# Kernel tuning notes

Measured on AMD Instinct MI355X. Metric: run time of the kernel, lower is better.

Reference implementation:

```python
import jax, jax.numpy as jnp
import numpy as np

EPS = 1e-5

def _ln(x):
    # LayerNorm without affine (elementwise_affine=False when adaLN=True)
    m = jnp.mean(x, axis=-1, keepdims=True)
    v = jnp.mean((x - m) ** 2, axis=-1, keepdims=True)
    return (x - m) / jnp.sqrt(v + EPS)

def _ln_affine(x, g, b):
    return _ln(x) * g + b

def setup_inputs() -> dict:
    key = jax.random.key(0)
    B, L, D, H, P = 2, 1024, 1024, 16, 64
    FF = 4 * D
    ks = jax.random.split(key, 16)
    s = 0.02
    inp = {
        'x': jax.random.normal(ks[0], (B, L, D), jnp.float32),
        'z': jax.random.normal(ks[1], (B, L, L, P), jnp.float32),
        'trans': jax.random.normal(ks[2], (B, L, 3), jnp.float32),
        'mask': jnp.ones((B, L), jnp.bool_),
        'x_cond': jax.random.normal(ks[3], (B, L, D), jnp.float32),
        # adaLN modulation: SiLU -> Linear(D, 6D). (Randomly init'd; the torch
        # code zero-inits it, which would zero the whole block output.)
        'ada_W': jax.random.normal(ks[4], (D, 6 * D), jnp.float32) * s,
        'ada_b': jnp.zeros((6 * D,), jnp.float32),
        # attention projections (torch Linear weights stored as [in, out])
        'Wq': jax.random.normal(ks[5], (D, D), jnp.float32) * s,
        'bq': jnp.zeros((D,), jnp.float32),
        'Wk': jax.random.normal(ks[6], (D, D), jnp.float32) * s,
        'bk': jnp.zeros((D,), jnp.float32),
        'Wv': jax.random.normal(ks[7], (D, D), jnp.float32) * s,
        'bv': jnp.zeros((D,), jnp.float32),
        'Wo': jax.random.normal(ks[8], (D, D), jnp.float32) * s,
        'bo': jnp.zeros((D,), jnp.float32),
        # FeedForward: LayerNorm(D) (affine) -> Linear(D,FF) -> ReLU -> Linear(FF,D)
        'ln_g': jnp.ones((D,), jnp.float32),
        'ln_b': jnp.zeros((D,), jnp.float32),
        'W1': jax.random.normal(ks[9], (D, FF), jnp.float32) * s,
        'b1': jnp.zeros((FF,), jnp.float32),
        'W2': jax.random.normal(ks[10], (FF, D), jnp.float32) * s,
        'b2': jnp.zeros((D,), jnp.float32),
    }
    return inp

def _block(x, z, trans, mask, x_cond, ada_W, ada_b, Wq, bq, Wk, bk, Wv, bv,
           Wo, bo, ln_g, ln_b, W1, b1, W2, b2):
    B, L, D = x.shape
    H = 16
    dh = D // H
    # adaLN modulation from conditioning signal
    c = jax.nn.silu(x_cond) @ ada_W + ada_b
    (shift_mha, scale_mha, gate_mha,
     shift_mlp, scale_mlp, gate_mlp) = jnp.split(c, 6, axis=-1)
    # --- attention branch: norm -> modulate -> MHA -> gate -> residual ---
    h = _ln(x) * (1.0 + scale_mha) + shift_mha
    q = (h @ Wq + bq).reshape(B, L, H, dh)
    k = (h @ Wk + bk).reshape(B, L, H, dh)
    v = (h @ Wv + bv).reshape(B, L, H, dh)
    scores = jnp.einsum('blhd,bmhd->bhlm', q, k) / jnp.sqrt(jnp.float32(dh))
    neg = jnp.finfo(scores.dtype).min
    scores = jnp.where(mask[:, None, None, :], scores, neg)
    attn = jax.nn.softmax(scores, axis=-1)
    o = jnp.einsum('bhlm,bmhd->blhd', attn, v).reshape(B, L, D)
    mha_out = o @ Wo + bo
    x = x + mha_out * gate_mha
    # --- FFN branch: norm -> modulate -> FF(LN, Lin, ReLU, Lin) -> gate ---
    h = _ln(x) * (1.0 + scale_mlp) + shift_mlp
    h = _ln_affine(h, ln_g, ln_b)
    h = jax.nn.relu(h @ W1 + b1)
    ff_out = h @ W2 + b2
    x = x + ff_out * gate_mlp
    # pair_updates=False, frame_update=False: z and trans pass through
    return x, z, trans

def reference(x, z, trans, mask, x_cond, ada_W, ada_b, Wq, bq, Wk, bk, Wv, bv,
              Wo, bo, ln_g, ln_b, W1, b1, W2, b2):
    return _block(x, z, trans, mask, x_cond, ada_W, ada_b, Wq, bq, Wk, bk,
                  Wv, bv, Wo, bo, ln_g, ln_b, W1, b1, W2, b2)
```

## Files before the change

### kernel.cpp

```cpp
#include <hip/hip_runtime.h>
#include <hip/hip_bf16.h>


typedef __attribute__((ext_vector_type(8))) __bf16 bf16x8;
typedef __attribute__((ext_vector_type(4))) float f32x4;
typedef __attribute__((ext_vector_type(8))) unsigned short ushortx8;

#define DEVI static __device__ __forceinline__

DEVI unsigned short f2bf(float f) {
    __hip_bfloat16 h = __float2bfloat16(f);
    return __builtin_bit_cast(unsigned short, h);
}

DEVI void gload16(const void* g, void* l) {
    __builtin_amdgcn_global_load_lds(
        (const __attribute__((address_space(1))) void*)g,
        (__attribute__((address_space(3))) void*)l, 16, 0, 0);
}

DEVI void side_copy(const float4* __restrict__ src, float4* __restrict__ dst,
                    long long len, long long cb, long long ncb) {
    const long long nthr = ncb * 256;
    for (long long i = cb * 256 + threadIdx.x; i < len; i += nthr)
        dst[i] = src[i];
}

__global__ __launch_bounds__(256) void transpose_cast(
        const float* __restrict__ in, unsigned short* __restrict__ out,
        int K, int N) {
    __shared__ float tile[32][33];
    const int n0 = blockIdx.x * 32, k0 = blockIdx.y * 32;
    const int tx = threadIdx.x, ty = threadIdx.y;
#pragma unroll
    for (int i = 0; i < 4; ++i)
        tile[ty + 8 * i][tx] = in[(size_t)(k0 + ty + 8 * i) * N + n0 + tx];
    __syncthreads();
#pragma unroll
    for (int i = 0; i < 4; ++i)
        out[(size_t)(n0 + ty + 8 * i) * K + k0 + tx] = f2bf(tile[tx][ty + 8 * i]);
}

__global__ __launch_bounds__(256) void silu_cast(
        const float* __restrict__ x, unsigned short* __restrict__ o) {
    const int i = blockIdx.x * 256 + threadIdx.x;
    float4 v = ((const float4*)x)[i];
    ushort4 r;
    r.x = f2bf(v.x / (1.f + __expf(-v.x)));
    r.y = f2bf(v.y / (1.f + __expf(-v.y)));
    r.z = f2bf(v.z / (1.f + __expf(-v.z)));
    r.w = f2bf(v.w / (1.f + __expf(-v.w)));
    ((ushort4*)o)[i] = r;
}

__global__ void concat3(const float* __restrict__ a, const float* __restrict__ b,
                        const float* __restrict__ c, float* __restrict__ o, int D) {
    const int i = blockIdx.x * 256 + threadIdx.x;
    if (i < D) o[i] = a[i];
    else if (i < 2 * D) o[i] = b[i - D];
    else if (i < 3 * D) o[i] = c[i - 2 * D];
}

template <int MODE, int MT>
__global__ __launch_bounds__(256) void gemm_bt(
        const unsigned short* __restrict__ A, const unsigned short* __restrict__ Bt,
        const float* __restrict__ bias,
        float* __restrict__ outf, unsigned short* __restrict__ outb,
        const float* __restrict__ res, const float* __restrict__ gate, int gstride,
        int M, int N, int K,
        unsigned short* __restrict__ vt, int twoD, int H, int Lr) {
    __shared__ __align__(16) unsigned short lA[MT * 32 * 32];
    __shared__ __align__(16) unsigned short lB[128 * 32];
    const int tid = threadIdx.x;
    const int wave = tid >> 6, lane = tid & 63;
    const int fr = lane & 15, fg = lane >> 4;
    const int wr = wave >> 1, wc = wave & 1;
    const int m0 = blockIdx.y * (MT * 32), n0 = blockIdx.x * 128;

    f32x4 acc[MT][4];
#pragma unroll
    for (int i = 0; i < MT; ++i)
#pragma unroll
        for (int j = 0; j < 4; ++j) acc[i][j] = (f32x4){0.f, 0.f, 0.f, 0.f};

    for (int k0 = 0; k0 < K; k0 += 32) {
#pragma unroll
        for (int ch = 0; ch < 2; ++ch) {
            const int p = ch * 4096 + wave * 1024 + lane * 16;
            const int row = p >> 6, kb = p & 63;
            if (ch < MT / 2)
                gload16((const char*)A + ((size_t)(m0 + row) * K + k0) * 2 + kb, (char*)lA + p);
            gload16((const char*)Bt + ((size_t)(n0 + row) * K + k0) * 2 + kb, (char*)lB + p);
        }
        __syncthreads();
        bf16x8 af[MT], bfm[4];
#pragma unroll
        for (int t = 0; t < MT; ++t)
            af[t] = *(const bf16x8*)((const char*)lA + ((wr * (MT * 16) + t * 16 + fr) * 32 + fg * 8) * 2);
#pragma unroll
        for (int t = 0; t < 4; ++t)
            bfm[t] = *(const bf16x8*)((const char*)lB + ((wc * 64 + t * 16 + fr) * 32 + fg * 8) * 2);
#pragma unroll
        for (int mt = 0; mt < MT; ++mt)
#pragma unroll
            for (int nt = 0; nt < 4; ++nt)
                acc[mt][nt] = __builtin_amdgcn_mfma_f32_16x16x32_bf16(
                        af[mt], bfm[nt], acc[mt][nt], 0, 0, 0);
        __syncthreads();
    }
#pragma unroll
    for (int mt = 0; mt < MT; ++mt)
#pragma unroll
        for (int nt = 0; nt < 4; ++nt) {
            const int gcol = n0 + wc * 64 + nt * 16 + fr;
            const float bb = bias[gcol];
#pragma unroll
            for (int j = 0; j < 4; ++j) {
                const int grow = m0 + wr * (MT * 16) + mt * 16 + fg * 4 + j;
                const size_t idx = (size_t)grow * N + gcol;
                const float v = acc[mt][nt][j] + bb;
                if constexpr (MODE == 0) outf[idx] = v;
                else if constexpr (MODE == 1) outb[idx] = f2bf(v);
                else if constexpr (MODE == 2) outf[idx] = res[idx] + v * gate[(size_t)grow * gstride + gcol];
                else if constexpr (MODE == 3) outb[idx] = f2bf(fmaxf(v, 0.f));
                else {
                    const unsigned short bv16 = f2bf(v);
                    outb[idx] = bv16;
                    if (gcol >= twoD) {
                        const int d = gcol - twoD, hh = d >> 6, dd = d & 63;
                        const int bb2 = grow >= Lr ? 1 : 0, l = grow - bb2 * Lr;
                        vt[((size_t)(bb2 * H + hh) * 64 + dd) * Lr + l] = bv16;
                    }
                }
            }
        }
}

__global__ __launch_bounds__(256) void ln_mod(
        const float* __restrict__ x, const float* __restrict__ c,
        unsigned short* __restrict__ h, int D, int cs) {
    const int row = blockIdx.x, tid = threadIdx.x;
    const int lane = tid & 63, wave = tid >> 6;
    const float4 xv = ((const float4*)(x + (size_t)row * D))[tid];
    float s = xv.x + xv.y + xv.z + xv.w;
    float ss = xv.x * xv.x + xv.y * xv.y + xv.z * xv.z + xv.w * xv.w;
#pragma unroll
    for (int o = 1; o < 64; o <<= 1) { s += __shfl_xor(s, o); ss += __shfl_xor(ss, o); }
    __shared__ float red[8];
    if (lane == 0) { red[wave] = s; red[4 + wave] = ss; }
    __syncthreads();
    s = red[0] + red[1] + red[2] + red[3];
    ss = red[4] + red[5] + red[6] + red[7];
    const float mean = s / D;
    const float rstd = rsqrtf(ss / D - mean * mean + 1e-5f);
    const float* crow = c + (size_t)row * cs;
    const float4 sh = ((const float4*)(crow))[tid];
    const float4 sc = ((const float4*)(crow + D))[tid];
    ushort4 r;
    r.x = f2bf((xv.x - mean) * rstd * (1.f + sc.x) + sh.x);
    r.y = f2bf((xv.y - mean) * rstd * (1.f + sc.y) + sh.y);
    r.z = f2bf((xv.z - mean) * rstd * (1.f + sc.z) + sh.z);
    r.w = f2bf((xv.w - mean) * rstd * (1.f + sc.w) + sh.w);
    ((ushort4*)(h + (size_t)row * D))[tid] = r;
}

__global__ __launch_bounds__(256) void ln2_mod(
        const float* __restrict__ x2, const float* __restrict__ c,
        const float* __restrict__ g, const float* __restrict__ bb,
        unsigned short* __restrict__ h, int D, int cs) {
    const int row = blockIdx.x, tid = threadIdx.x;
    const int lane = tid & 63, wave = tid >> 6;
    const float4 xv = ((const float4*)(x2 + (size_t)row * D))[tid];
    float s = xv.x + xv.y + xv.z + xv.w;
    float ss = xv.x * xv.x + xv.y * xv.y + xv.z * xv.z + xv.w * xv.w;
#pragma unroll
    for (int o = 1; o < 64; o <<= 1) { s += __shfl_xor(s, o); ss += __shfl_xor(ss, o); }
    __shared__ float red[16];
    if (lane == 0) { red[wave] = s; red[4 + wave] = ss; }
    __syncthreads();
    s = red[0] + red[1] + red[2] + red[3];
    ss = red[4] + red[5] + red[6] + red[7];
    const float mean = s / D;
    const float rstd = rsqrtf(ss / D - mean * mean + 1e-5f);
    const float* crow = c + (size_t)row * cs;
    const float4 sh = ((const float4*)(crow + 3 * D))[tid];
    const float4 sc = ((const float4*)(crow + 4 * D))[tid];
    float t[4];
    t[0] = (xv.x - mean) * rstd * (1.f + sc.x) + sh.x;
    t[1] = (xv.y - mean) * rstd * (1.f + sc.y) + sh.y;
    t[2] = (xv.z - mean) * rstd * (1.f + sc.z) + sh.z;
    t[3] = (xv.w - mean) * rstd * (1.f + sc.w) + sh.w;
    float s2 = t[0] + t[1] + t[2] + t[3];
    float ss2 = t[0] * t[0] + t[1] * t[1] + t[2] * t[2] + t[3] * t[3];
#pragma unroll
    for (int o = 1; o < 64; o <<= 1) { s2 += __shfl_xor(s2, o); ss2 += __shfl_xor(ss2, o); }
    if (lane == 0) { red[8 + wave] = s2; red[12 + wave] = ss2; }
    __syncthreads();
    s2 = red[8] + red[9] + red[10] + red[11];
    ss2 = red[12] + red[13] + red[14] + red[15];
    const float mean2 = s2 / D;
    const float rstd2 = rsqrtf(ss2 / D - mean2 * mean2 + 1e-5f);
    const float4 gv = ((const float4*)g)[tid];
    const float4 bv = ((const float4*)bb)[tid];
    ushort4 r;
    r.x = f2bf((t[0] - mean2) * rstd2 * gv.x + bv.x);
    r.y = f2bf((t[1] - mean2) * rstd2 * gv.y + bv.y);
    r.z = f2bf((t[2] - mean2) * rstd2 * gv.z + bv.z);
    r.w = f2bf((t[3] - mean2) * rstd2 * gv.w + bv.w);
    ((ushort4*)(h + (size_t)row * D))[tid] = r;
}

__global__ __launch_bounds__(256) void attn_fwd(
        const unsigned short* __restrict__ qkv, const unsigned short* __restrict__ vt,
        unsigned short* __restrict__ o,
        int L, int D, int B,
        const float4* __restrict__ cp_src, float4* __restrict__ cp_dst,
        long long cp_len) {
    if ((int)blockIdx.z >= B) {
        const long long cb = (long long)(blockIdx.z - B) * gridDim.x * gridDim.y
                           + (long long)blockIdx.y * gridDim.x + blockIdx.x;
        const long long ncb = (long long)(gridDim.z - B) * gridDim.x * gridDim.y;
        side_copy(cp_src, cp_dst, cp_len, cb, ncb);
        return;
    }
    const int q0 = blockIdx.x * 64, hh = blockIdx.y, b = blockIdx.z;
    const int H = gridDim.y;
    const int tid = threadIdx.x, wave = tid >> 6, lane = tid & 63;
    const int fr = lane & 15, fg = lane >> 4;
    const size_t rs = 3 * (size_t)D;
    const unsigned short* vtb = vt + (size_t)(b * H + hh) * 64 * L;
    __shared__ __align__(16) unsigned short lK[64 * 72];
    __shared__ __align__(16) unsigned short lVT[64 * 72];
    __shared__ __align__(16) unsigned short lP[4 * 16 * 72];

    bf16x8 aq[2];
    {
        const size_t qr = (size_t)(b * L + q0 + wave * 16 + fr);
#pragma unroll
        for (int kk = 0; kk < 2; ++kk)
            aq[kk] = *(const bf16x8*)(qkv + qr * rs + hh * 64 + kk * 32 + fg * 8);
    }
    f32x4 oacc[4];
#pragma unroll
    for (int i = 0; i < 4; ++i) oacc[i] = (f32x4){0.f, 0.f, 0.f, 0.f};
    float m_run[4] = {-1e30f, -1e30f, -1e30f, -1e30f};
    float l_run[4] = {0.f, 0.f, 0.f, 0.f};

    for (int n0 = 0; n0 < L; n0 += 64) {
        __syncthreads();
#pragma unroll
        for (int it = 0; it < 2; ++it) {
            const int idx = it * 256 + tid, r = idx >> 3, cc = idx & 7;
            const unsigned short* src = qkv + (size_t)(b * L + n0 + r) * rs + D + hh * 64 + cc * 8;
            *(ushortx8*)(&lK[r * 72 + cc * 8]) = *(const ushortx8*)src;
        }
#pragma unroll
        for (int it = 0; it < 2; ++it) {
            const int idx = it * 256 + tid, r = idx >> 3, cc = idx & 7;
            *(ushortx8*)(&lVT[r * 72 + cc * 8]) =
                *(const ushortx8*)(vtb + (size_t)r * L + n0 + cc * 8);
        }
        __syncthreads();
        f32x4 sfr[4];
#pragma unroll
        for (int nt = 0; nt < 4; ++nt) {
            const bf16x8 bk0 = *(const bf16x8*)((const char*)lK + ((nt * 16 + fr) * 72 + fg * 8) * 2);
            const bf16x8 bk1 = *(const bf16x8*)((const char*)lK + ((nt * 16 + fr) * 72 + 32 + fg * 8) * 2);
            f32x4 t = (f32x4){0.f, 0.f, 0.f, 0.f};
            t = __builtin_amdgcn_mfma_f32_16x16x32_bf16(aq[0], bk0, t, 0, 0, 0);
            t = __builtin_amdgcn_mfma_f32_16x16x32_bf16(aq[1], bk1, t, 0, 0, 0);
#pragma unroll
            for (int j = 0; j < 4; ++j) t[j] *= 0.125f;
            sfr[nt] = t;
        }
        float tm[4], prs[4], alpha[4];
#pragma unroll
        for (int j = 0; j < 4; ++j) {
            float v = fmaxf(fmaxf(sfr[0][j], sfr[1][j]), fmaxf(sfr[2][j], sfr[3][j]));
#pragma unroll
            for (int off = 1; off < 16; off <<= 1) v = fmaxf(v, __shfl_xor(v, off));
            tm[j] = v;
        }
#pragma unroll
        for (int j = 0; j < 4; ++j) {
            const float mn = fmaxf(m_run[j], tm[j]);
            alpha[j] = __expf(m_run[j] - mn);
            m_run[j] = mn;
            prs[j] = 0.f;
        }
#pragma unroll
        for (int nt = 0; nt < 4; ++nt)
#pragma unroll
            for (int j = 0; j < 4; ++j) {
                const float p = __expf(sfr[nt][j] - m_run[j]);
                sfr[nt][j] = p;
                prs[j] += p;
            }
#pragma unroll
        for (int j = 0; j < 4; ++j) {
#pragma unroll
            for (int off = 1; off < 16; off <<= 1) prs[j] += __shfl_xor(prs[j], off);
            l_run[j] = l_run[j] * alpha[j] + prs[j];
        }
#pragma unroll
        for (int dt = 0; dt < 4; ++dt)
#pragma unroll
            for (int j = 0; j < 4; ++j) oacc[dt][j] *= alpha[j];
        unsigned short* pw = &lP[wave * 16 * 72];
#pragma unroll
        for (int nt = 0; nt < 4; ++nt)
#pragma unroll
            for (int j = 0; j < 4; ++j)
                pw[(fg * 4 + j) * 72 + nt * 16 + fr] = f2bf(sfr[nt][j]);
        const bf16x8 ap0 = *(const bf16x8*)((const char*)pw + (fr * 72 + fg * 8) * 2);
        const bf16x8 ap1 = *(const bf16x8*)((const char*)pw + (fr * 72 + 32 + fg * 8) * 2);
#pragma unroll
        for (int dt = 0; dt < 4; ++dt) {
            const bf16x8 bv0 = *(const bf16x8*)((const char*)lVT + ((dt * 16 + fr) * 72 + fg * 8) * 2);
            const bf16x8 bv1 = *(const bf16x8*)((const char*)lVT + ((dt * 16 + fr) * 72 + 32 + fg * 8) * 2);
            oacc[dt] = __builtin_amdgcn_mfma_f32_16x16x32_bf16(ap0, bv0, oacc[dt], 0, 0, 0);
            oacc[dt] = __builtin_amdgcn_mfma_f32_16x16x32_bf16(ap1, bv1, oacc[dt], 0, 0, 0);
        }
    }
    float inv[4];
#pragma unroll
    for (int j = 0; j < 4; ++j) inv[j] = 1.f / l_run[j];
#pragma unroll
    for (int dt = 0; dt < 4; ++dt)
#pragma unroll
        for (int j = 0; j < 4; ++j) {
            const int orow = b * L + q0 + wave * 16 + fg * 4 + j;
            o[(size_t)orow * D + hh * 64 + dt * 16 + fr] = f2bf(oacc[dt][j] * inv[j]);
        }
}

extern "C" void kernel_launch(void* const* d_in, const int* in_sizes, int n_in,
                              void* d_out, int out_size, void* d_ws, size_t ws_size,
                              hipStream_t stream) {
    (void)n_in; (void)out_size;
    const float* x      = (const float*)d_in[0];
    const float* z      = (const float*)d_in[1];
    const float* trans  = (const float*)d_in[2];
    const float* x_cond = (const float*)d_in[4];
    const float* ada_W  = (const float*)d_in[5];
    const float* ada_b  = (const float*)d_in[6];
    const float* Wq = (const float*)d_in[7];  const float* bq = (const float*)d_in[8];
    const float* Wk = (const float*)d_in[9];  const float* bk = (const float*)d_in[10];
    const float* Wv = (const float*)d_in[11]; const float* bv = (const float*)d_in[12];
    const float* Wo = (const float*)d_in[13]; const float* bo = (const float*)d_in[14];
    const float* ln_g = (const float*)d_in[15]; const float* ln_b = (const float*)d_in[16];
    const float* W1 = (const float*)d_in[17]; const float* b1 = (const float*)d_in[18];
    const float* W2 = (const float*)d_in[19]; const float* b2 = (const float*)d_in[20];

    const int D  = in_sizes[6] / 6;
    const int FF = in_sizes[18];
    const int M  = in_sizes[0] / D;
    const int B  = 2, L = M / B, H = 16;
    const size_t zN = (size_t)in_sizes[1], tN = (size_t)in_sizes[2];

    float* out_x = (float*)d_out;
    float* out_z = out_x + (size_t)M * D;
    float* out_t = out_z + zN;

    size_t off = 0;
    auto alloc = [&](size_t bytes) { size_t o = off; off += (bytes + 255) & ~(size_t)255; return o; };
    const size_t o_adaWt = alloc((size_t)6 * D * D * 2);
    const size_t o_Wqkvt = alloc((size_t)3 * D * D * 2);
    const size_t o_Wot   = alloc((size_t)D * D * 2);
    const size_t o_W1t   = alloc((size_t)FF * D * 2);
    const size_t o_W2t   = alloc((size_t)D * FF * 2);
    const size_t o_bqkv  = alloc((size_t)3 * D * 4);
    const size_t o_xcb   = alloc((size_t)M * D * 2);
    const size_t o_c     = alloc((size_t)M * 6 * D * 4);
    const size_t o_hb    = alloc((size_t)M * D * 2);
    const size_t o_qkv   = alloc((size_t)M * 3 * D * 2);
    const size_t o_vt    = alloc((size_t)M * D * 2);
    const size_t o_ob    = alloc((size_t)M * D * 2);
    const size_t o_x2    = alloc((size_t)M * D * 4);
    const size_t o_h2b   = alloc((size_t)M * D * 2);
    const size_t o_f1    = alloc((size_t)M * FF * 2);
    const size_t need = off;
    const bool have_ws = (ws_size >= need);
    char* base = have_ws ? (char*)d_ws : (char*)out_z;

    unsigned short* adaWt = (unsigned short*)(base + o_adaWt);
    unsigned short* Wqkvt = (unsigned short*)(base + o_Wqkvt);
    unsigned short* Wot   = (unsigned short*)(base + o_Wot);
    unsigned short* W1t   = (unsigned short*)(base + o_W1t);
    unsigned short* W2t   = (unsigned short*)(base + o_W2t);
    float*          bqkv  = (float*)(base + o_bqkv);
    unsigned short* xcb   = (unsigned short*)(base + o_xcb);
    float*          cbuf  = (float*)(base + o_c);
    unsigned short* hb    = (unsigned short*)(base + o_hb);
    unsigned short* qkvb  = (unsigned short*)(base + o_qkv);
    unsigned short* vtb   = (unsigned short*)(base + o_vt);
    unsigned short* ob    = (unsigned short*)(base + o_ob);
    float*          x2    = (float*)(base + o_x2);
    unsigned short* h2b   = (unsigned short*)(base + o_h2b);
    unsigned short* f1b   = (unsigned short*)(base + o_f1);

    const float4* zs = (const float4*)z;
    float4* zd = (float4*)out_z;
    const long long zN4 = (long long)(zN / 4);
    const int ECOPY = have_ws ? 6 : 0;
    const long long cplen = have_ws ? zN4 : 0;

    const dim3 tb(32, 8);
    transpose_cast<<<dim3(6 * D / 32, D / 32), tb, 0, stream>>>(ada_W, adaWt, D, 6 * D);
    transpose_cast<<<dim3(D / 32, D / 32), tb, 0, stream>>>(Wq, Wqkvt, D, D);
    transpose_cast<<<dim3(D / 32, D / 32), tb, 0, stream>>>(Wk, Wqkvt + (size_t)D * D, D, D);
    transpose_cast<<<dim3(D / 32, D / 32), tb, 0, stream>>>(Wv, Wqkvt + (size_t)2 * D * D, D, D);
    transpose_cast<<<dim3(D / 32, D / 32), tb, 0, stream>>>(Wo, Wot, D, D);
    transpose_cast<<<dim3(FF / 32, D / 32), tb, 0, stream>>>(W1, W1t, D, FF);
    transpose_cast<<<dim3(D / 32, FF / 32), tb, 0, stream>>>(W2, W2t, FF, D);
    concat3<<<(3 * D + 255) / 256, 256, 0, stream>>>(bq, bk, bv, bqkv, D);
    silu_cast<<<M * D / 1024, 256, 0, stream>>>(x_cond, xcb);

    const int gy128 = M / 128, gy64 = M / 64;
    gemm_bt<0, 4><<<dim3(6 * D / 128, gy128), 256, 0, stream>>>(
            xcb, adaWt, ada_b, cbuf, nullptr, nullptr, nullptr, 0, M, 6 * D, D,
            nullptr, 0, 0, 0);
    ln_mod<<<M, 256, 0, stream>>>(x, cbuf, hb, D, 6 * D);
    gemm_bt<4, 4><<<dim3(3 * D / 128, gy128), 256, 0, stream>>>(
            hb, Wqkvt, bqkv, nullptr, qkvb, nullptr, nullptr, 0, M, 3 * D, D,
            vtb, 2 * D, H, L);
    attn_fwd<<<dim3(L / 64, H, B + ECOPY), 256, 0, stream>>>(qkvb, vtb, ob, L, D, B,
            zs, zd, cplen);
    gemm_bt<2, 2><<<dim3(D / 128, gy64), 256, 0, stream>>>(
            ob, Wot, bo, x2, nullptr, x, cbuf + 2 * D, 6 * D, M, D, D,
            nullptr, 0, 0, 0);
    ln2_mod<<<M, 256, 0, stream>>>(x2, cbuf, ln_g, ln_b, h2b, D, 6 * D);
    gemm_bt<3, 4><<<dim3(FF / 128, gy128), 256, 0, stream>>>(
            h2b, W1t, b1, nullptr, f1b, nullptr, nullptr, 0, M, FF, D,
            nullptr, 0, 0, 0);
    gemm_bt<2, 2><<<dim3(D / 128, gy64), 256, 0, stream>>>(
            f1b, W2t, b2, out_x, nullptr, x2, cbuf + 5 * D, 6 * D, M, D, FF,
            nullptr, 0, 0, 0);

    if (!have_ws) {
        hipMemcpyAsync(out_z, z, zN * 4, hipMemcpyDeviceToDevice, stream);
    }
    hipMemcpyAsync(out_t, trans, tN * 4, hipMemcpyDeviceToDevice, stream);
}
```

Baseline: 1.213 ms.

## Fuse prep kernels into one launch and spread z copy across GEMMs

Merges the seven weight transpose-casts, the SiLU cast and the bias concat into a single prep_all launch to cut launch overhead. It also splits the large z pass-through copy (512 MB) into three parts: one half stays in attention, and the other parts ride as extra blocks on the FF1 and FF2 GEMMs so they overlap with compute. The risk is that the copy blocks compete for bandwidth and CUs with the GEMM tiles, and that the uneven split leaves some kernels longer.

```diff
diff --git a/kernel.cpp b/kernel.cpp
--- a/kernel.cpp
+++ b/kernel.cpp
@@ -20,45 +20,75 @@
 }
 
 DEVI void side_copy(const float4* __restrict__ src, float4* __restrict__ dst,
-                    long long len, long long cb, long long ncb) {
+                    long long off, long long len, long long cb, long long ncb) {
     const long long nthr = ncb * 256;
     for (long long i = cb * 256 + threadIdx.x; i < len; i += nthr)
-        dst[i] = src[i];
-}
-
-__global__ __launch_bounds__(256) void transpose_cast(
-        const float* __restrict__ in, unsigned short* __restrict__ out,
-        int K, int N) {
+        dst[off + i] = src[off + i];
+}
+
+__global__ __launch_bounds__(256) void prep_all(
+        const float* __restrict__ adaW, const float* __restrict__ Wq,
+        const float* __restrict__ Wk, const float* __restrict__ Wv,
+        const float* __restrict__ Wo, const float* __restrict__ W1,
+        const float* __restrict__ W2,
+        const float* __restrict__ bq, const float* __restrict__ bk,
+        const float* __restrict__ bv, const float* __restrict__ xc,
+        unsigned short* __restrict__ adaWt, unsigned short* __restrict__ Wqkvt,
+        unsigned short* __restrict__ Wot, unsigned short* __restrict__ W1t,
+        unsigned short* __restrict__ W2t, float* __restrict__ bqkv,
+        unsigned short* __restrict__ xcb, int D, int FF, int M) {
+    const int tx = threadIdx.x, ty = threadIdx.y;
+    const int tAda = (6 * D / 32) * (D / 32);
+    const int tSq  = (D / 32) * (D / 32);
+    const int tW1  = (FF / 32) * (D / 32);
+    const int tW2  = (D / 32) * (FF / 32);
+    const int nT = tAda + 4 * tSq + tW1 + tW2;
+    const int sb = M * D / 1024;
+    int b = blockIdx.x;
     __shared__ float tile[32][33];
-    const int n0 = blockIdx.x * 32, k0 = blockIdx.y * 32;
-    const int tx = threadIdx.x, ty = threadIdx.y;
+    if (b >= nT) {
+        int r = b - nT;
+        const int tid = ty * 32 + tx;
+        if (r < sb) {
+            const int i = r * 256 + tid;
+            float4 v = ((const float4*)xc)[i];
+            ushort4 o;
+            o.x = f2bf(v.x / (1.f + __expf(-v.x)));
+            o.y = f2bf(v.y / (1.f + __expf(-v.y)));
+            o.z = f2bf(v.z / (1.f + __expf(-v.z)));
+            o.w = f2bf(v.w / (1.f + __expf(-v.w)));
+            ((ushort4*)xcb)[i] = o;
+        } else {
+            const int i = (r - sb) * 256 + tid;
+            if (i < D) bqkv[i] = bq[i];
+            else if (i < 2 * D) bqkv[i] = bk[i - D];
+            else if (i < 3 * D) bqkv[i] = bv[i - 2 * D];
+        }
+        return;
+    }
+    const float* src; unsigned short* dst; int K, N;
+    if (b < tAda) { src = adaW; dst = adaWt; K = D; N = 6 * D; }
+    else { b -= tAda;
+      if (b < tSq) { src = Wq; dst = Wqkvt; K = D; N = D; }
+      else { b -= tSq;
+        if (b < tSq) { src = Wk; dst = Wqkvt + (size_t)D * D; K = D; N = D; }
+        else { b -= tSq;
+          if (b < tSq) { src = Wv; dst = Wqkvt + (size_t)2 * D * D; K = D; N = D; }
+          else { b -= tSq;
+            if (b < tSq) { src = Wo; dst = Wot; K = D; N = D; }
+            else { b -= tSq;
+              if (b < tW1) { src = W1; dst = W1t; K = D; N = FF; }
+              else { b -= tW1; src = W2; dst = W2t; K = FF; N = D; }
+            }}}}}
+    const int ntx = N / 32;
+    const int n0 = (b % ntx) * 32, k0 = (b / ntx) * 32;
 #pragma unroll
     for (int i = 0; i < 4; ++i)
-        tile[ty + 8 * i][tx] = in[(size_t)(k0 + ty + 8 * i) * N + n0 + tx];
+        tile[ty + 8 * i][tx] = src[(size_t)(k0 + ty + 8 * i) * N + n0 + tx];
     __syncthreads();
 #pragma unroll
     for (int i = 0; i < 4; ++i)
-        out[(size_t)(n0 + ty + 8 * i) * K + k0 + tx] = f2bf(tile[tx][ty + 8 * i]);
-}
-
-__global__ __launch_bounds__(256) void silu_cast(
-        const float* __restrict__ x, unsigned short* __restrict__ o) {
-    const int i = blockIdx.x * 256 + threadIdx.x;
-    float4 v = ((const float4*)x)[i];
-    ushort4 r;
-    r.x = f2bf(v.x / (1.f + __expf(-v.x)));
-    r.y = f2bf(v.y / (1.f + __expf(-v.y)));
-    r.z = f2bf(v.z / (1.f + __expf(-v.z)));
-    r.w = f2bf(v.w / (1.f + __expf(-v.w)));
-    ((ushort4*)o)[i] = r;
-}
-
-__global__ void concat3(const float* __restrict__ a, const float* __restrict__ b,
-                        const float* __restrict__ c, float* __restrict__ o, int D) {
-    const int i = blockIdx.x * 256 + threadIdx.x;
-    if (i < D) o[i] = a[i];
-    else if (i < 2 * D) o[i] = b[i - D];
-    else if (i < 3 * D) o[i] = c[i - 2 * D];
+        dst[(size_t)(n0 + ty + 8 * i) * K + k0 + tx] = f2bf(tile[tx][ty + 8 * i]);
 }
 
 template <int MODE, int MT>
@@ -68,7 +98,15 @@
         float* __restrict__ outf, unsigned short* __restrict__ outb,
         const float* __restrict__ res, const float* __restrict__ gate, int gstride,
         int M, int N, int K,
-        unsigned short* __restrict__ vt, int twoD, int H, int Lr) {
+        unsigned short* __restrict__ vt, int twoD, int H, int Lr,
+        const float4* __restrict__ cp_src, float4* __restrict__ cp_dst,
+        long long cp_off, long long cp_len, int gy) {
+    if ((int)blockIdx.y >= gy) {
+        const long long cb = (long long)(blockIdx.y - gy) * gridDim.x + blockIdx.x;
+        const long long ncb = (long long)(gridDim.y - gy) * gridDim.x;
+        side_copy(cp_src, cp_dst, cp_off, cp_len, cb, ncb);
+        return;
+    }
     __shared__ __align__(16) unsigned short lA[MT * 32 * 32];
     __shared__ __align__(16) unsigned short lB[128 * 32];
     const int tid = threadIdx.x;
@@ -215,12 +253,12 @@
         unsigned short* __restrict__ o,
         int L, int D, int B,
         const float4* __restrict__ cp_src, float4* __restrict__ cp_dst,
-        long long cp_len) {
+        long long cp_off, long long cp_len) {
     if ((int)blockIdx.z >= B) {
         const long long cb = (long long)(blockIdx.z - B) * gridDim.x * gridDim.y
                            + (long long)blockIdx.y * gridDim.x + blockIdx.x;
         const long long ncb = (long long)(gridDim.z - B) * gridDim.x * gridDim.y;
-        side_copy(cp_src, cp_dst, cp_len, cb, ncb);
+        side_copy(cp_src, cp_dst, cp_off, cp_len, cb, ncb);
         return;
     }
     const int q0 = blockIdx.x * 64, hh = blockIdx.y, b = blockIdx.z;
@@ -403,39 +441,45 @@
     float4* zd = (float4*)out_z;
     const long long zN4 = (long long)(zN / 4);
     const int ECOPY = have_ws ? 6 : 0;
-    const long long cplen = have_ws ? zN4 : 0;
-
-    const dim3 tb(32, 8);
-    transpose_cast<<<dim3(6 * D / 32, D / 32), tb, 0, stream>>>(ada_W, adaWt, D, 6 * D);
-    transpose_cast<<<dim3(D / 32, D / 32), tb, 0, stream>>>(Wq, Wqkvt, D, D);
-    transpose_cast<<<dim3(D / 32, D / 32), tb, 0, stream>>>(Wk, Wqkvt + (size_t)D * D, D, D);
-    transpose_cast<<<dim3(D / 32, D / 32), tb, 0, stream>>>(Wv, Wqkvt + (size_t)2 * D * D, D, D);
-    transpose_cast<<<dim3(D / 32, D / 32), tb, 0, stream>>>(Wo, Wot, D, D);
-    transpose_cast<<<dim3(FF / 32, D / 32), tb, 0, stream>>>(W1, W1t, D, FF);
-    transpose_cast<<<dim3(D / 32, FF / 32), tb, 0, stream>>>(W2, W2t, FF, D);
-    concat3<<<(3 * D + 255) / 256, 256, 0, stream>>>(bq, bk, bv, bqkv, D);
-    silu_cast<<<M * D / 1024, 256, 0, stream>>>(x_cond, xcb);
+    const int eF1 = have_ws ? 24 : 0;
+    const int eF2 = have_ws ? 96 : 0;
+    const long long cA  = have_ws ? zN4 / 2 : 0;
+    const long long cF1 = have_ws ? zN4 / 4 : 0;
+    const long long cF2 = have_ws ? zN4 - cA - cF1 : 0;
+
+    {
+        const int tAda = (6 * D / 32) * (D / 32);
+        const int tSq  = (D / 32) * (D / 32);
+        const int tW1  = (FF / 32) * (D / 32);
+        const int tW2  = (D / 32) * (FF / 32);
+        const int nT = tAda + 4 * tSq + tW1 + tW2;
+        const int sb = M * D / 1024;
+        const int cbk = (3 * D + 255) / 256;
+        prep_all<<<nT + sb + cbk, dim3(32, 8), 0, stream>>>(
+                ada_W, Wq, Wk, Wv, Wo, W1, W2, bq, bk, bv, x_cond,
+                adaWt, Wqkvt, Wot, W1t, W2t, bqkv, xcb, D, FF, M);
+    }
 
     const int gy128 = M / 128, gy64 = M / 64;
     gemm_bt<0, 4><<<dim3(6 * D / 128, gy128), 256, 0, stream>>>(
             xcb, adaWt, ada_b, cbuf, nullptr, nullptr, nullptr, 0, M, 6 * D, D,
-            nullptr, 0, 0, 0);
+            nullptr, 0, 0, 0, nullptr, nullptr, 0, 0, gy128);
     ln_mod<<<M, 256, 0, stream>>>(x, cbuf, hb, D, 6 * D);
     gemm_bt<4, 4><<<dim3(3 * D / 128, gy128), 256, 0, stream>>>(
             hb, Wqkvt, bqkv, nullptr, qkvb, nullptr, nullptr, 0, M, 3 * D, D,
-            vtb, 2 * D, H, L);
+            vtb, 2 * D, H, L, nullptr, nullptr, 0, 0, gy128);
     attn_fwd<<<dim3(L / 64, H, B + ECOPY), 256, 0, stream>>>(qkvb, vtb, ob, L, D, B,
-            zs, zd, cplen);
+            zs, zd, 0, cA);
     gemm_bt<2, 2><<<dim3(D / 128, gy64), 256, 0, stream>>>(
             ob, Wot, bo, x2, nullptr, x, cbuf + 2 * D, 6 * D, M, D, D,
-            nullptr, 0, 0, 0);
+            nullptr, 0, 0, 0, nullptr, nullptr, 0, 0, gy64);
     ln2_mod<<<M, 256, 0, stream>>>(x2, cbuf, ln_g, ln_b, h2b, D, 6 * D);
-    gemm_bt<3, 4><<<dim3(FF / 128, gy128), 256, 0, stream>>>(
+    gemm_bt<3, 4><<<dim3(FF / 128, gy128 + eF1), 256, 0, stream>>>(
             h2b, W1t, b1, nullptr, f1b, nullptr, nullptr, 0, M, FF, D,
-            nullptr, 0, 0, 0);
-    gemm_bt<2, 2><<<dim3(D / 128, gy64), 256, 0, stream>>>(
+            nullptr, 0, 0, 0, zs, zd, cA, cF1, gy128);
+    gemm_bt<2, 2><<<dim3(D / 128, gy64 + eF2), 256, 0, stream>>>(
             f1b, W2t, b2, out_x, nullptr, x2, cbuf + 5 * D, 6 * D, M, D, FF,
-            nullptr, 0, 0, 0);
+            nullptr, 0, 0, 0, zs, zd, cA + cF1, cF2, gy64);
 
     if (!have_ws) {
         hipMemcpyAsync(out_z, z, zN * 4, hipMemcpyDeviceToDevice, stream);
```

After: 1.156 ms. 4.7% less time.
